# Kernel tuning notes

Hardware: AMD Instinct MI355X
Metric: run time of the kernel (lower is better)

Reference implementation:

```python
import jax, jax.numpy as jnp
import numpy as np

NEG_SLOPE = 0.2


def add_self_loops(edge_index, num_nodes):
    loop = jnp.arange(num_nodes, dtype=edge_index.dtype)
    loops = jnp.stack([loop, loop])  # [2, N]
    return jnp.concatenate([edge_index, loops], axis=1)


def gat_conv(x, edge_index, W, a_src, a_dst, b, concat=True):
    """PyG-style GATConv. a_src/a_dst: [1, H, C]. W: [F_in, H*C]."""
    N = x.shape[0]
    H, C = a_src.shape[1], a_src.shape[2]
    xp = (x @ W).reshape(N, H, C)                       # [N, H, C]
    alpha_src = (xp * a_src).sum(-1)                    # [N, H]
    alpha_dst = (xp * a_dst).sum(-1)                    # [N, H]
    src, dst = edge_index[0], edge_index[1]
    e = alpha_src[src] + alpha_dst[dst]                 # [E, H]
    e = jnp.where(e > 0, e, NEG_SLOPE * e)              # LeakyReLU(0.2)
    # per-destination segment softmax
    m = jax.ops.segment_max(e, dst, num_segments=N)     # [N, H]
    m = jnp.where(jnp.isfinite(m), m, 0.0)
    ez = jnp.exp(e - m[dst])
    s = jax.ops.segment_sum(ez, dst, num_segments=N)    # [N, H]
    alpha = ez / (s[dst] + 1e-16)                       # [E, H]
    msg = xp[src] * alpha[:, :, None]                   # [E, H, C]
    out = jax.ops.segment_sum(msg, dst, num_segments=N) # [N, H, C]
    out = out.reshape(N, H * C) if concat else out.mean(axis=1)
    return out + b


def setup_inputs() -> dict:
    key = jax.random.key(0)
    ks = jax.random.split(key, 16)
    N, F, E, CLS = 100000, 256, 1600000, 10
    x = jax.random.normal(ks[0], (N, F), dtype=jnp.float32)
    edge_index = jax.random.randint(ks[1], (2, E), 0, N, dtype=jnp.int64)

    def glorot(k, shape):
        fan = shape[0] + shape[-1] * (shape[1] if len(shape) == 3 else 1)
        return jax.random.uniform(k, shape, jnp.float32, -1.0, 1.0) * jnp.sqrt(6.0 / fan)

    return {
        "x": x, "edge_index": edge_index,
        "W1": glorot(ks[2], (F, 128)),  "a1s": glorot(ks[3], (1, 8, 16)),
        "a1d": glorot(ks[4], (1, 8, 16)), "b1": jnp.zeros((128,), jnp.float32),
        "W2": glorot(ks[5], (128, 64)), "a2s": glorot(ks[6], (1, 8, 8)),
        "a2d": glorot(ks[7], (1, 8, 8)),  "b2": jnp.zeros((64,), jnp.float32),
        "W3": glorot(ks[8], (64, CLS)), "a3s": glorot(ks[9], (1, 1, CLS)),
        "a3d": glorot(ks[10], (1, 1, CLS)), "b3": jnp.zeros((CLS,), jnp.float32),
    }


def reference(x, edge_index, W1, a1s, a1d, b1, W2, a2s, a2d, b2, W3, a3s, a3d, b3):
    ei = add_self_loops(edge_index, x.shape[0])
    h = jax.nn.elu(gat_conv(x, ei, W1, a1s, a1d, b1))
    h = jax.nn.elu(gat_conv(h, ei, W2, a2s, a2d, b2))
    h = gat_conv(h, ei, W3, a3s, a3d, b3)
    return jax.nn.log_softmax(h, axis=1)
```

## Files before the change

### kernel.cpp

```cpp
#include <hip/hip_runtime.h>
#include <hip/hip_bf16.h>
#include <math.h>


#define LEAKY(v) ((v) > 0.f ? (v) : 0.2f * (v))

typedef __bf16 bf16_t;
typedef __bf16 bf16x8 __attribute__((ext_vector_type(8)));
typedef __bf16 bf16x4 __attribute__((ext_vector_type(4)));
typedef float f32x4 __attribute__((ext_vector_type(4)));
typedef unsigned short u16x8 __attribute__((ext_vector_type(8)));

static __device__ __forceinline__ unsigned short bf_bits(float f) {
    bf16_t b = (bf16_t)f;
    return __builtin_bit_cast(unsigned short, b);
}
static __device__ __forceinline__ float bf_to_f(unsigned short u) {
    return __uint_as_float(((unsigned int)u) << 16);
}
static __device__ __forceinline__ float bperm_f(int byteaddr, float v) {
    return __uint_as_float((unsigned)__builtin_amdgcn_ds_bpermute(byteaddr, (int)__float_as_uint(v)));
}

constexpr int NB_MAX = 400;
constexpr int BCAP = 5120;

__global__ __launch_bounds__(256) void partition_k(
        const int* __restrict__ src, const int* __restrict__ dst, int E, int NB,
        int* __restrict__ bcur, unsigned* __restrict__ staged) {
    __shared__ int hist[NB_MAX];
    __shared__ int bstart[NB_MAX + 1];
    __shared__ int cur[NB_MAX];
    __shared__ int gbase[NB_MAX];
    __shared__ unsigned words[4096];
    __shared__ unsigned short bidl[4096];
    int tid = threadIdx.x;
    int e0 = blockIdx.x * 4096;
    int cnt = E - e0; if (cnt > 4096) cnt = 4096;
    if (cnt <= 0) return;

    for (int b = tid; b < NB; b += 256) hist[b] = 0;
    __syncthreads();
    for (int i = tid; i < cnt; i += 256) atomicAdd(&hist[dst[e0 + i] >> 8], 1);
    __syncthreads();
    if (tid < 64) {
        int lane = tid;
        int run = 0;
        for (int b0 = 0; b0 < NB; b0 += 64) {
            int bb = b0 + lane;
            int v = (bb < NB) ? hist[bb] : 0;
            int sc = v;
            for (int off = 1; off < 64; off <<= 1) {
                int t2 = __shfl_up(sc, off, 64);
                if (lane >= off) sc += t2;
            }
            if (bb < NB) bstart[bb] = run + sc - v;
            run += __shfl(sc, 63, 64);
        }
        if (lane == 0) bstart[NB] = run;
    }
    __syncthreads();
    for (int b = tid; b < NB; b += 256) {
        cur[b] = bstart[b];
        gbase[b] = hist[b] ? atomicAdd(&bcur[b], hist[b]) : 0;
    }
    __syncthreads();
    for (int i = tid; i < cnt; i += 256) {
        int s = src[e0 + i], d = dst[e0 + i];
        int b = d >> 8;
        unsigned w = (unsigned)s | ((unsigned)(d & 255) << 17);
        int p = atomicAdd(&cur[b], 1);
        words[p] = w;
        bidl[p] = (unsigned short)b;
    }
    __syncthreads();
    for (int i = tid; i < cnt; i += 256) {
        int b = bidl[i];
        staged[(size_t)b * BCAP + gbase[b] + (i - bstart[b])] = words[i];
    }
}

__global__ __launch_bounds__(256) void buildcsr_k(
        const unsigned* __restrict__ staged, const int* __restrict__ bcur,
        int* __restrict__ offs, int* __restrict__ cols,
        int N, int NB) {
    __shared__ int h[256], hs[256], curl[256];
    __shared__ int colsl[BCAP];
    __shared__ int base_s;
    int b = blockIdx.x, tid = threadIdx.x;
    int n0 = b << 8;
    int ecnt = bcur[b];
    const unsigned* sb = staged + (size_t)b * BCAP;

    h[tid] = 0;
    if (tid < 64) {
        int acc2 = 0;
        for (int i = tid; i < b; i += 64) acc2 += bcur[i];
        for (int off = 1; off < 64; off <<= 1) acc2 += __shfl_xor(acc2, off, 64);
        if (tid == 0) base_s = acc2;
    }
    __syncthreads();
    int base_g = base_s;
    for (int i = tid; i < ecnt; i += 256) atomicAdd(&h[sb[i] >> 17], 1);
    __syncthreads();
    int val = h[tid];
    hs[tid] = val; __syncthreads();
    for (int off = 1; off < 256; off <<= 1) {
        int t = (tid >= off) ? hs[tid - off] : 0;
        __syncthreads();
        hs[tid] += t;
        __syncthreads();
    }
    int excl = hs[tid] - val;
    curl[tid] = excl;
    if (n0 + tid < N) offs[n0 + tid] = base_g + excl;
    if (b == NB - 1 && tid == 0) offs[N] = base_g + ecnt;
    __syncthreads();
    for (int i = tid; i < ecnt; i += 256) {
        unsigned w = sb[i];
        int p = atomicAdd(&curl[w >> 17], 1);
        colsl[p] = (int)(w & 0x1FFFFu);
    }
    __syncthreads();
    for (int i = tid; i < ecnt; i += 256) cols[base_g + i] = colsl[i];
}

static __device__ __forceinline__ void prep_w_dev(
        const float* __restrict__ W, short* __restrict__ Bfs,
        int K, int N, int NT, int idx) {
    int lane = idx & 63;
    int t = idx >> 6;
    int ntile = t % NT, kstep = t / NT;
    int quad = lane >> 4, nl = lane & 15;
    int n = ntile * 16 + nl;
    bf16_t* dst = (bf16_t*)Bfs + (size_t)idx * 16;
#pragma unroll
    for (int j = 0; j < 8; j++) {
        int k = kstep * 32 + quad * 8 + j;
        float v = W[k * N + n];
        bf16_t h = (bf16_t)v;
        bf16_t l = (bf16_t)(v - (float)h);
        dst[j] = h;
        dst[8 + j] = l;
    }
}
static __device__ __forceinline__ void prep_w3_dev(
        const float* __restrict__ W, short* __restrict__ Bfs, int Nc, int idx) {
    int lane = idx & 63, ks = idx >> 6;
    int quad = lane >> 4, nl = lane & 15;
    bf16_t* dst = (bf16_t*)Bfs + (size_t)idx * 16;
#pragma unroll
    for (int j = 0; j < 8; j++) {
        int k = ks * 32 + quad * 8 + j;
        float v = (nl < Nc) ? W[k * Nc + nl] : 0.f;
        bf16_t h = (bf16_t)v;
        bf16_t l = (bf16_t)(v - (float)h);
        dst[j] = h;
        dst[8 + j] = l;
    }
}
__global__ void prep_all_k(const float* __restrict__ W1, const float* __restrict__ W2,
                           const float* __restrict__ W3, short* __restrict__ Bf1,
                           short* __restrict__ Bf2, short* __restrict__ Bf3) {
    int idx = blockIdx.x * blockDim.x + threadIdx.x;
    if (idx < 4096) prep_w_dev(W1, Bf1, 256, 128, 8, idx);
    else if (idx < 5120) prep_w_dev(W2, Bf2, 128, 64, 4, idx - 4096);
    else if (idx < 5248) prep_w3_dev(W3, Bf3, 10, idx - 5120);
}

template <int BM, int WMT, int WNT, int NWM, bool ABF16, int CHEAD, int K>
__global__ __launch_bounds__(256, 2) void mfma_gemm_k(
        const void* __restrict__ Av, const short* __restrict__ Bfs,
        unsigned short* __restrict__ Cb,
        const float* __restrict__ a_s, const float* __restrict__ a_d,
        float* __restrict__ out_as, float* __restrict__ out_ad,
        int M, int N, int NT) {
    constexpr int NWN = 4 / NWM;
    constexpr int BN = 16 * WNT * NWN;
    constexpr int KP = K + 8;
    constexpr int BNP = BN + 2;
    constexpr size_t ASZ = (size_t)BM * KP * 2 * (ABF16 ? 1 : 2);
    constexpr size_t CSZ = (size_t)BM * BNP * 4;
    constexpr size_t SMEM = ASZ > CSZ ? ASZ : CSZ;
    __shared__ __align__(16) char smem[SMEM];
    bf16_t* As_hi = (bf16_t*)smem;
    bf16_t* As_lo = As_hi + (ABF16 ? 0 : (size_t)BM * KP);
    float* Ct = (float*)smem;
    const bf16_t* Bf = (const bf16_t*)Bfs;

    int tid = threadIdx.x;
    int wave = tid >> 6, lane = tid & 63;
    int quad = lane >> 4, l16 = lane & 15;
    int wm = wave % NWM, wn = wave / NWM;
    int row0 = blockIdx.x * BM;
    int ntile0 = blockIdx.y * (BN / 16) + wn * WNT;

    if constexpr (!ABF16) {
        constexpr int CHUNKS = BM * K * 4 / (16 * 256);
        const float* A = (const float*)Av;
        f32x4 tmp[CHUNKS];
#pragma unroll
        for (int c = 0; c < CHUNKS; c++) {
            int ci = c * 256 + tid;
            int fi = ci * 4;
            int row = fi / K, k = fi % K;
            int grow = row0 + row;
            tmp[c] = (f32x4){0.f, 0.f, 0.f, 0.f};
            if (grow < M) tmp[c] = *(const f32x4*)(A + (size_t)grow * K + k);
        }
#pragma unroll
        for (int c = 0; c < CHUNKS; c++) {
            int ci = c * 256 + tid;
            int fi = ci * 4;
            int row = fi / K, k = fi % K;
            bf16x4 h, l;
#pragma unroll
            for (int j = 0; j < 4; j++) {
                bf16_t hh = (bf16_t)tmp[c][j];
                h[j] = hh;
                l[j] = (bf16_t)(tmp[c][j] - (float)hh);
            }
            *(bf16x4*)&As_hi[row * KP + k] = h;
            *(bf16x4*)&As_lo[row * KP + k] = l;
        }
    } else {
        constexpr int CHUNKS = BM * K * 2 / (16 * 256);
        const unsigned short* A = (const unsigned short*)Av;
        u16x8 tmp[CHUNKS];
#pragma unroll
        for (int c = 0; c < CHUNKS; c++) {
            int ci = c * 256 + tid;
            int ei = ci * 8;
            int row = ei / K, k = ei % K;
            int grow = row0 + row;
            tmp[c] = (u16x8){0, 0, 0, 0, 0, 0, 0, 0};
            if (grow < M) tmp[c] = *(const u16x8*)(A + (size_t)grow * K + k);
        }
#pragma unroll
        for (int c = 0; c < CHUNKS; c++) {
            int ci = c * 256 + tid;
            int ei = ci * 8;
            int row = ei / K, k = ei % K;
            *(u16x8*)&As_hi[row * KP + k] = tmp[c];
        }
    }
    __syncthreads();

    f32x4 acc[WMT][WNT];
#pragma unroll
    for (int i = 0; i < WMT; i++)
#pragma unroll
        for (int j = 0; j < WNT; j++) acc[i][j] = (f32x4){0.f, 0.f, 0.f, 0.f};

#pragma unroll
    for (int ks = 0; ks < K / 32; ks++) {
        bf16x8 ah[WMT], al[WMT];
#pragma unroll
        for (int i = 0; i < WMT; i++) {
            int rowl = wm * (WMT * 16) + i * 16 + l16;
            ah[i] = *(const bf16x8*)&As_hi[rowl * KP + ks * 32 + quad * 8];
            if (!ABF16) al[i] = *(const bf16x8*)&As_lo[rowl * KP + ks * 32 + quad * 8];
        }
        bf16x8 bh[WNT], bl[WNT];
#pragma unroll
        for (int j = 0; j < WNT; j++) {
            size_t base = ((size_t)(ks * NT + ntile0 + j) * 64 + lane) * 16;
            bh[j] = *(const bf16x8*)&Bf[base];
            bl[j] = *(const bf16x8*)&Bf[base + 8];
        }
#pragma unroll
        for (int i = 0; i < WMT; i++)
#pragma unroll
            for (int j = 0; j < WNT; j++) {
                acc[i][j] = __builtin_amdgcn_mfma_f32_16x16x32_bf16(ah[i], bh[j], acc[i][j], 0, 0, 0);
                if (!ABF16)
                    acc[i][j] = __builtin_amdgcn_mfma_f32_16x16x32_bf16(al[i], bh[j], acc[i][j], 0, 0, 0);
                acc[i][j] = __builtin_amdgcn_mfma_f32_16x16x32_bf16(ah[i], bl[j], acc[i][j], 0, 0, 0);
            }
    }

    __syncthreads();
#pragma unroll
    for (int i = 0; i < WMT; i++) {
        int rbase = wm * (WMT * 16) + i * 16 + quad * 4;
#pragma unroll
        for (int j = 0; j < WNT; j++) {
            int lcol = (wn * WNT + j) * 16 + l16;
#pragma unroll
            for (int r2 = 0; r2 < 4; r2++)
                Ct[(size_t)(rbase + r2) * BNP + lcol] = acc[i][j][r2];
        }
    }
    __syncthreads();

    constexpr int HB = BN / CHEAD;
    const int colbase = blockIdx.y * BN;
    const int Hh = N / CHEAD;
#pragma unroll
    for (int o = 0; o < (BM * HB + 255) / 256; o++) {
        int idx = o * 256 + tid;
        if (idx < BM * HB) {
            int row = idx & (BM - 1);
            int hd = idx / BM;
            const float* crow = Ct + (size_t)row * BNP + hd * CHEAD;
            float ss = 0.f, sd = 0.f;
#pragma unroll
            for (int c = 0; c < CHEAD; c++) {
                float v = crow[c];
                ss = fmaf(v, a_s[colbase + hd * CHEAD + c], ss);
                sd = fmaf(v, a_d[colbase + hd * CHEAD + c], sd);
            }
            int grow = row0 + row;
            if (grow < M) {
                out_as[(size_t)grow * Hh + blockIdx.y * HB + hd] = ss;
                out_ad[(size_t)grow * Hh + blockIdx.y * HB + hd] = sd;
            }
        }
    }

    constexpr int CU2 = BM * BN / 2;
#pragma unroll
    for (int o = 0; o < CU2 / 256; o++) {
        int idx = o * 256 + tid;
        int row = idx / (BN / 2);
        int uc = idx - row * (BN / 2);
        float v0 = Ct[(size_t)row * BNP + uc * 2];
        float v1 = Ct[(size_t)row * BNP + uc * 2 + 1];
        unsigned pk = (unsigned)bf_bits(v0) | ((unsigned)bf_bits(v1) << 16);
        int grow = row0 + row;
        if (grow < M)
            ((unsigned*)Cb)[((size_t)grow * N + colbase) / 2 + uc] = pk;
    }
}

__global__ __launch_bounds__(256) void gemm3_k(
        const unsigned short* __restrict__ Ab, const short* __restrict__ Bfs,
        unsigned short* __restrict__ Cb,
        const float* __restrict__ a_s, const float* __restrict__ a_d,
        float* __restrict__ out_as, float* __restrict__ out_ad, int M) {
    const bf16_t* Bf = (const bf16_t*)Bfs;
    int tid = threadIdx.x;
    int wave = tid >> 6, lane = tid & 63;
    int quad = lane >> 4, l16 = lane & 15;
    int grow0 = blockIdx.x * 64 + wave * 16;

    bf16x8 bh[2], bl[2];
#pragma unroll
    for (int ks = 0; ks < 2; ks++) {
        size_t base = (size_t)(ks * 64 + lane) * 16;
        bh[ks] = *(const bf16x8*)&Bf[base];
        bl[ks] = *(const bf16x8*)&Bf[base + 8];
    }

    int arow = grow0 + l16; if (arow >= M) arow = M - 1;
    f32x4 acc = (f32x4){0.f, 0.f, 0.f, 0.f};
#pragma unroll
    for (int ks = 0; ks < 2; ks++) {
        bf16x8 a = *(const bf16x8*)(Ab + (size_t)arow * 64 + ks * 32 + quad * 8);
        acc = __builtin_amdgcn_mfma_f32_16x16x32_bf16(a, bh[ks], acc, 0, 0, 0);
        acc = __builtin_amdgcn_mfma_f32_16x16x32_bf16(a, bl[ks], acc, 0, 0, 0);
    }

    bool colv = l16 < 10;
    float cs = colv ? a_s[l16] : 0.f;
    float cd = colv ? a_d[l16] : 0.f;
    float ps[4], pd[4];
#pragma unroll
    for (int r = 0; r < 4; r++) { ps[r] = acc[r] * cs; pd[r] = acc[r] * cd; }
#pragma unroll
    for (int off = 1; off < 16; off <<= 1) {
#pragma unroll
        for (int r = 0; r < 4; r++) {
            ps[r] += __shfl_xor(ps[r], off, 64);
            pd[r] += __shfl_xor(pd[r], off, 64);
        }
    }
#pragma unroll
    for (int r = 0; r < 4; r++) {
        int grow = grow0 + quad * 4 + r;
        if (grow < M) {
            if (colv) Cb[(size_t)grow * 10 + l16] = bf_bits(acc[r]);
            if (l16 == 0) { out_as[grow] = ps[r]; out_ad[grow] = pd[r]; }
        }
    }
}

template <bool DO_ELU>
__global__ void agg16_k(const unsigned short* __restrict__ xpb,
                        const float* __restrict__ asrc, const float* __restrict__ adst,
                        const int* __restrict__ offs, const int* __restrict__ cols,
                        const float* __restrict__ bias, unsigned short* __restrict__ outb,
                        int N) {
    int gtid = blockIdx.x * blockDim.x + threadIdx.x;
    int n = gtid >> 6;
    if (n >= N) return;
    int lane = threadIdx.x & 63;
    int j = lane >> 3, h = lane & 7;
    const int jb = j << 2;
    int start = offs[n], end = offs[n + 1];
    const unsigned* xp32 = (const unsigned*)xpb;

    unsigned uself = xp32[(size_t)n * 64 + lane];
    float ad_l = adst[n * 8 + h];
    float vs = asrc[n * 8 + h] + ad_l;
    vs = LEAKY(vs);

    float m_w = vs;
    float s = (j == 0) ? 1.f : 0.f;
    float m_f = bperm_f(jb, vs);
    float a0 = __uint_as_float(uself << 16);
    float a1 = __uint_as_float(uself & 0xffff0000u);

    for (int c0 = start; c0 < end; c0 += 16) {
        int e0 = c0 + j, e1 = c0 + 8 + j;
        bool ok0 = e0 < end, ok1 = e1 < end;
        int sl0 = ok0 ? cols[e0] : 0;
        int sl1 = ok1 ? cols[e1] : 0;
        unsigned u[16];
#pragma unroll
        for (int t = 0; t < 8; t++) {
            int srcj = __builtin_amdgcn_readlane(sl0, t * 8);
            u[t] = xp32[(size_t)srcj * 64 + lane];
        }
#pragma unroll
        for (int t = 0; t < 8; t++) {
            int srcj = __builtin_amdgcn_readlane(sl1, t * 8);
            u[8 + t] = xp32[(size_t)srcj * 64 + lane];
        }
        float v0 = -1e30f, v1 = -1e30f;
        if (ok0) { v0 = asrc[sl0 * 8 + h] + ad_l; v0 = LEAKY(v0); }
        if (ok1) { v1 = asrc[sl1 * 8 + h] + ad_l; v1 = LEAKY(v1); }
        float cm = fmaxf(v0, v1);
        cm = fmaxf(cm, __shfl_xor(cm, 8, 64));
        cm = fmaxf(cm, __shfl_xor(cm, 16, 64));
        cm = fmaxf(cm, __shfl_xor(cm, 32, 64));
        float mw_new = fmaxf(m_w, cm);
        float w0 = __expf(v0 - mw_new);
        float w1 = __expf(v1 - mw_new);
        s = s * __expf(m_w - mw_new) + w0 + w1;
        m_w = mw_new;
        float cmF = bperm_f(jb, cm);
        float mf_new = fmaxf(m_f, cmF);
        float scF = __expf(m_f - mf_new);
        m_f = mf_new;
        a0 *= scF; a1 *= scF;
        float wl[16];
#pragma unroll
        for (int t = 0; t < 8; t++) wl[t] = bperm_f(jb + t * 32, w0);
#pragma unroll
        for (int t = 0; t < 8; t++) wl[8 + t] = bperm_f(jb + t * 32, w1);
#pragma unroll
        for (int t = 0; t < 16; t++) {
            a0 = fmaf(wl[t], __uint_as_float(u[t] << 16), a0);
            a1 = fmaf(wl[t], __uint_as_float(u[t] & 0xffff0000u), a1);
        }
    }
    s += __shfl_xor(s, 8, 64);
    s += __shfl_xor(s, 16, 64);
    s += __shfl_xor(s, 32, 64);
    float rs = 1.f / (s + 1e-16f);
    float rsF = bperm_f(jb, rs);
    float o0 = a0 * rsF + bias[2 * lane];
    float o1 = a1 * rsF + bias[2 * lane + 1];
    if (DO_ELU) {
        o0 = o0 > 0.f ? o0 : __expf(o0) - 1.f;
        o1 = o1 > 0.f ? o1 : __expf(o1) - 1.f;
    }
    unsigned packed = (unsigned)bf_bits(o0) | ((unsigned)bf_bits(o1) << 16);
    ((unsigned*)outb)[(size_t)n * 64 + lane] = packed;
}

template <bool DO_ELU>
__global__ void agg8c8_k(const unsigned short* __restrict__ xpb,
                         const float* __restrict__ asrc, const float* __restrict__ adst,
                         const int* __restrict__ offs, const int* __restrict__ cols,
                         const float* __restrict__ bias, unsigned short* __restrict__ outb,
                         int N) {
    int gtid = blockIdx.x * blockDim.x + threadIdx.x;
    int n = gtid >> 6;
    if (n >= N) return;
    int lane = threadIdx.x & 63;
    int j = lane >> 3, h = lane & 7;
    int start = offs[n], end = offs[n + 1];
    const unsigned* xp32 = (const unsigned*)xpb;

    int fp = lane & 31;
    int hF = fp >> 2;
    int half = lane >> 5;
    int sbase = half * 32;

    float ad_l = adst[n * 8 + h];
    float vs = asrc[n * 8 + h] + ad_l;
    vs = LEAKY(vs);

    float m_w = vs;
    float s = (j == 0) ? 1.f : 0.f;
    float m_f = bperm_f(hF * 4, vs);
    float a0 = 0.f, a1 = 0.f;
    if (half == 0) {
        unsigned u = xp32[(size_t)n * 32 + fp];
        a0 = __uint_as_float(u << 16);
        a1 = __uint_as_float(u & 0xffff0000u);
    }

    for (int c0 = start; c0 < end; c0 += 16) {
        int e0 = c0 + j, e1 = c0 + 8 + j;
        bool ok0 = e0 < end, ok1 = e1 < end;
        int sl0 = ok0 ? cols[e0] : 0;
        int sl1 = ok1 ? cols[e1] : 0;
        int sv[8];
#pragma unroll
        for (int t = 0; t < 4; t++) sv[t] = __builtin_amdgcn_ds_bpermute(sbase + t * 64, sl0);
#pragma unroll
        for (int t = 0; t < 4; t++) sv[4 + t] = __builtin_amdgcn_ds_bpermute(sbase + t * 64, sl1);
        unsigned u[8];
#pragma unroll
        for (int t = 0; t < 8; t++) u[t] = xp32[(size_t)sv[t] * 32 + fp];
        float v0 = -1e30f, v1 = -1e30f;
        if (ok0) { v0 = asrc[sl0 * 8 + h] + ad_l; v0 = LEAKY(v0); }
        if (ok1) { v1 = asrc[sl1 * 8 + h] + ad_l; v1 = LEAKY(v1); }
        float cm = fmaxf(v0, v1);
        cm = fmaxf(cm, __shfl_xor(cm, 8, 64));
        cm = fmaxf(cm, __shfl_xor(cm, 16, 64));
        cm = fmaxf(cm, __shfl_xor(cm, 32, 64));
        float mw_new = fmaxf(m_w, cm);
        float w0 = __expf(v0 - mw_new);
        float w1 = __expf(v1 - mw_new);
        s = s * __expf(m_w - mw_new) + w0 + w1;
        m_w = mw_new;
        float cmF = bperm_f(hF * 4, cm);
        float mf_new = fmaxf(m_f, cmF);
        float scF = __expf(m_f - mf_new);
        m_f = mf_new;
        a0 *= scF; a1 *= scF;
        float wl[8];
#pragma unroll
        for (int t = 0; t < 4; t++) wl[t] = bperm_f(sbase + hF * 4 + t * 64, w0);
#pragma unroll
        for (int t = 0; t < 4; t++) wl[4 + t] = bperm_f(sbase + hF * 4 + t * 64, w1);
#pragma unroll
        for (int t = 0; t < 8; t++) {
            a0 = fmaf(wl[t], __uint_as_float(u[t] << 16), a0);
            a1 = fmaf(wl[t], __uint_as_float(u[t] & 0xffff0000u), a1);
        }
    }
    s += __shfl_xor(s, 8, 64);
    s += __shfl_xor(s, 16, 64);
    s += __shfl_xor(s, 32, 64);
    float rs = 1.f / (s + 1e-16f);
    float rsF = bperm_f(hF * 4, rs);
    a0 += __shfl_xor(a0, 32, 64);
    a1 += __shfl_xor(a1, 32, 64);
    if (half == 0) {
        float o0 = a0 * rsF + bias[2 * fp];
        float o1 = a1 * rsF + bias[2 * fp + 1];
        if (DO_ELU) {
            o0 = o0 > 0.f ? o0 : __expf(o0) - 1.f;
            o1 = o1 > 0.f ? o1 : __expf(o1) - 1.f;
        }
        unsigned packed = (unsigned)bf_bits(o0) | ((unsigned)bf_bits(o1) << 16);
        ((unsigned*)outb)[(size_t)n * 32 + fp] = packed;
    }
}

__global__ void agg1h_k(const unsigned short* __restrict__ xpb,
                        const float* __restrict__ asrc, const float* __restrict__ adst,
                        const int* __restrict__ offs, const int* __restrict__ cols,
                        const float* __restrict__ bias, float* __restrict__ out, int N) {
    int gtid = blockIdx.x * blockDim.x + threadIdx.x;
    int n = gtid >> 6;
    if (n >= N) return;
    int lane = threadIdx.x & 63;
    int start = offs[n], end = offs[n + 1];
    float ad = adst[n];
    float vs = asrc[n] + ad;
    vs = LEAKY(vs);

    float m, s;
    if (lane == 0) { m = vs; s = 1.f; } else { m = -1e30f; s = 0.f; }
    for (int e = start + lane; e < end; e += 64) {
        float v = asrc[cols[e]] + ad;
        v = LEAKY(v);
        float mo = fmaxf(m, v);
        s = s * __expf(m - mo) + __expf(v - mo);
        m = mo;
    }
#pragma unroll
    for (int off = 1; off <= 32; off <<= 1) {
        float mo = __shfl_xor(m, off, 64);
        float so = __shfl_xor(s, off, 64);
        float mn = fmaxf(m, mo);
        s = s * __expf(m - mn) + so * __expf(mo - mn);
        m = mn;
    }
    float rs = 1.f / (s + 1e-16f);
    float wself = __expf(vs - m) * rs;

    int j = lane / 10, c = lane - j * 10;
    float acc = 0.f;
    if (j == 0) acc = wself * bf_to_f(xpb[(size_t)n * 10 + c]);
    for (int c0 = start; c0 < end; c0 += 6) {
        int e = c0 + j;
        if (j < 6 && e < end) {
            int src = cols[e];
            float v = asrc[src] + ad;
            v = LEAKY(v);
            float w = __expf(v - m) * rs;
            acc = fmaf(w, bf_to_f(xpb[(size_t)src * 10 + c]), acc);
        }
    }
    float tot = acc;
#pragma unroll
    for (int k = 1; k < 6; k++) tot += __shfl(acc, lane + 10 * k, 64);

    float z = tot + bias[lane < 10 ? lane : 0];
    float mx = -1e30f;
#pragma unroll
    for (int k = 0; k < 10; k++) mx = fmaxf(mx, __shfl(z, k, 64));
    float se = 0.f;
#pragma unroll
    for (int k = 0; k < 10; k++) se += __expf(__shfl(z, k, 64) - mx);
    if (lane < 10) out[(size_t)n * 10 + lane] = z - (__logf(se) + mx);
}


static inline size_t alignup(size_t x) { return (x + 255) & ~(size_t)255; }

extern "C" void kernel_launch(void* const* d_in, const int* in_sizes, int n_in,
                              void* d_out, int out_size, void* d_ws, size_t ws_size,
                              hipStream_t stream) {
    const float* x   = (const float*)d_in[0];
    const int*   ei  = (const int*)d_in[1];
    const float* W1  = (const float*)d_in[2];
    const float* a1s = (const float*)d_in[3];
    const float* a1d = (const float*)d_in[4];
    const float* b1  = (const float*)d_in[5];
    const float* W2  = (const float*)d_in[6];
    const float* a2s = (const float*)d_in[7];
    const float* a2d = (const float*)d_in[8];
    const float* b2  = (const float*)d_in[9];
    const float* W3  = (const float*)d_in[10];
    const float* a3s = (const float*)d_in[11];
    const float* a3d = (const float*)d_in[12];
    const float* b3  = (const float*)d_in[13];
    float* out = (float*)d_out;

    const int N = in_sizes[0] / 256;
    const int E = in_sizes[1] / 2;
    const int* src = ei;
    const int* dst = ei + E;
    const int NB = (N + 255) >> 8;

    char* p = (char*)d_ws;
    int* offs    = (int*)p; p += alignup(sizeof(int) * (size_t)(N + 1));
    int* bcur    = (int*)p; p += alignup(sizeof(int) * (size_t)(NB_MAX + 1));
    int* cols    = (int*)p; p += alignup(sizeof(int) * (size_t)E);
    unsigned short* xpb   = (unsigned short*)p; p += alignup(2 * (size_t)N * 128);
    unsigned short* hbufb = (unsigned short*)p; p += alignup(2 * (size_t)N * 128);
    float* xp    = (float*)p; p += alignup(sizeof(float) * (size_t)N * 128);
    float* as_   = (float*)p; p += alignup(sizeof(float) * (size_t)N * 8);
    float* ad_   = (float*)p; p += alignup(sizeof(float) * (size_t)N * 8);
    short* Bf1   = (short*)p; p += alignup(sizeof(short) * 8 * 8 * 64 * 16);
    short* Bf2   = (short*)p; p += alignup(sizeof(short) * 4 * 4 * 64 * 16);
    short* Bf3   = (short*)p; p += alignup(sizeof(short) * 2 * 1 * 64 * 16);
    unsigned* staged = (unsigned*)xp;

    const int TB = 256;

    hipMemsetAsync(bcur, 0, sizeof(int) * (size_t)(NB + 1), stream);
    partition_k<<<(E + 4095) / 4096, 256, 0, stream>>>(src, dst, E, NB, bcur, staged);
    buildcsr_k<<<NB, 256, 0, stream>>>(staged, bcur, offs, cols, N, NB);

    prep_all_k<<<(5248 + TB - 1) / TB, TB, 0, stream>>>(W1, W2, W3, Bf1, Bf2, Bf3);

    mfma_gemm_k<64, 4, 2, 1, false, 16, 256><<<dim3((N + 63) / 64, 1), 256, 0, stream>>>(
        x, Bf1, xpb, a1s, a1d, as_, ad_, N, 128, 8);
    agg16_k<true><<<(N * 64 + TB - 1) / TB, TB, 0, stream>>>(
        xpb, as_, ad_, offs, cols, b1, hbufb, N);

    mfma_gemm_k<64, 4, 1, 1, true, 8, 128><<<dim3((N + 63) / 64, 1), 256, 0, stream>>>(
        hbufb, Bf2, xpb, a2s, a2d, as_, ad_, N, 64, 4);
    agg8c8_k<true><<<(N * 64 + TB - 1) / TB, TB, 0, stream>>>(
        xpb, as_, ad_, offs, cols, b2, hbufb, N);

    gemm3_k<<<(N + 63) / 64, 256, 0, stream>>>(
        hbufb, Bf3, xpb, a3s, a3d, as_, ad_, N);
    agg1h_k<<<(N * 64 + TB - 1) / TB, TB, 0, stream>>>(
        xpb, as_, ad_, offs, cols, b3, out, N);
}
```

Baseline: 477.2 us.

## Fuse weight prep into partition and CSR build with layer-1 GEMM

Weight-split prep blocks now ride in the partition kernel's launch, and the CSR build blocks share one launch with the layer-1 GEMM blocks, so the two independent jobs overlap and two launches disappear. The layer-1 GEMM stages its A tile in two K-phases, which halves shared memory and allows three blocks per CU. The cost is an extra barrier and reload per phase, and CSR blocks now share a launch with a larger shared-memory footprint.

```diff
diff --git a/kernel.cpp b/kernel.cpp
--- a/kernel.cpp
+++ b/kernel.cpp
@@ -25,9 +25,47 @@
 constexpr int NB_MAX = 400;
 constexpr int BCAP = 5120;
 
-__global__ __launch_bounds__(256) void partition_k(
+static __device__ __forceinline__ void prep_w_dev(
+        const float* __restrict__ W, short* __restrict__ Bfs,
+        int K, int N, int NT, int idx) {
+    int lane = idx & 63;
+    int t = idx >> 6;
+    int ntile = t % NT, kstep = t / NT;
+    int quad = lane >> 4, nl = lane & 15;
+    int n = ntile * 16 + nl;
+    bf16_t* dst = (bf16_t*)Bfs + (size_t)idx * 16;
+#pragma unroll
+    for (int j = 0; j < 8; j++) {
+        int k = kstep * 32 + quad * 8 + j;
+        float v = W[k * N + n];
+        bf16_t h = (bf16_t)v;
+        bf16_t l = (bf16_t)(v - (float)h);
+        dst[j] = h;
+        dst[8 + j] = l;
+    }
+}
+static __device__ __forceinline__ void prep_w3_dev(
+        const float* __restrict__ W, short* __restrict__ Bfs, int Nc, int idx) {
+    int lane = idx & 63, ks = idx >> 6;
+    int quad = lane >> 4, nl = lane & 15;
+    bf16_t* dst = (bf16_t*)Bfs + (size_t)idx * 16;
+#pragma unroll
+    for (int j = 0; j < 8; j++) {
+        int k = ks * 32 + quad * 8 + j;
+        float v = (nl < Nc) ? W[k * Nc + nl] : 0.f;
+        bf16_t h = (bf16_t)v;
+        bf16_t l = (bf16_t)(v - (float)h);
+        dst[j] = h;
+        dst[8 + j] = l;
+    }
+}
+
+__global__ __launch_bounds__(256) void part_prep_k(
         const int* __restrict__ src, const int* __restrict__ dst, int E, int NB,
-        int* __restrict__ bcur, unsigned* __restrict__ staged) {
+        int* __restrict__ bcur, unsigned* __restrict__ staged, int PB,
+        const float* __restrict__ W1, const float* __restrict__ W2,
+        const float* __restrict__ W3, short* __restrict__ Bf1,
+        short* __restrict__ Bf2, short* __restrict__ Bf3) {
     __shared__ int hist[NB_MAX];
     __shared__ int bstart[NB_MAX + 1];
     __shared__ int cur[NB_MAX];
@@ -35,6 +73,15 @@
     __shared__ unsigned words[4096];
     __shared__ unsigned short bidl[4096];
     int tid = threadIdx.x;
+
+    if ((int)blockIdx.x >= PB) {
+        int idx = ((int)blockIdx.x - PB) * 256 + tid;
+        if (idx < 4096) prep_w_dev(W1, Bf1, 256, 128, 8, idx);
+        else if (idx < 5120) prep_w_dev(W2, Bf2, 128, 64, 4, idx - 4096);
+        else if (idx < 5248) prep_w3_dev(W3, Bf3, 10, idx - 5120);
+        return;
+    }
+
     int e0 = blockIdx.x * 4096;
     int cnt = E - e0; if (cnt > 4096) cnt = 4096;
     if (cnt <= 0) return;
@@ -80,14 +127,15 @@
     }
 }
 
-__global__ __launch_bounds__(256) void buildcsr_k(
-        const unsigned* __restrict__ staged, const int* __restrict__ bcur,
-        int* __restrict__ offs, int* __restrict__ cols,
-        int N, int NB) {
-    __shared__ int h[256], hs[256], curl[256];
-    __shared__ int colsl[BCAP];
-    __shared__ int base_s;
-    int b = blockIdx.x, tid = threadIdx.x;
+static __device__ void buildcsr_body(
+        char* smem, const unsigned* __restrict__ staged, const int* __restrict__ bcur,
+        int* __restrict__ offs, int* __restrict__ cols, int N, int NB, int b) {
+    int* h    = (int*)smem;
+    int* hs   = h + 256;
+    int* curl = hs + 256;
+    int* colsl = curl + 256;
+    int* base_p = colsl + BCAP;
+    int tid = threadIdx.x;
     int n0 = b << 8;
     int ecnt = bcur[b];
     const unsigned* sb = staged + (size_t)b * BCAP;
@@ -97,10 +145,10 @@
         int acc2 = 0;
         for (int i = tid; i < b; i += 64) acc2 += bcur[i];
         for (int off = 1; off < 64; off <<= 1) acc2 += __shfl_xor(acc2, off, 64);
-        if (tid == 0) base_s = acc2;
-    }
-    __syncthreads();
-    int base_g = base_s;
+        if (tid == 0) *base_p = acc2;
+    }
+    __syncthreads();
+    int base_g = *base_p;
     for (int i = tid; i < ecnt; i += 256) atomicAdd(&h[sb[i] >> 17], 1);
     __syncthreads();
     int val = h[tid];
@@ -125,66 +173,21 @@
     for (int i = tid; i < ecnt; i += 256) cols[base_g + i] = colsl[i];
 }
 
-static __device__ __forceinline__ void prep_w_dev(
-        const float* __restrict__ W, short* __restrict__ Bfs,
-        int K, int N, int NT, int idx) {
-    int lane = idx & 63;
-    int t = idx >> 6;
-    int ntile = t % NT, kstep = t / NT;
-    int quad = lane >> 4, nl = lane & 15;
-    int n = ntile * 16 + nl;
-    bf16_t* dst = (bf16_t*)Bfs + (size_t)idx * 16;
-#pragma unroll
-    for (int j = 0; j < 8; j++) {
-        int k = kstep * 32 + quad * 8 + j;
-        float v = W[k * N + n];
-        bf16_t h = (bf16_t)v;
-        bf16_t l = (bf16_t)(v - (float)h);
-        dst[j] = h;
-        dst[8 + j] = l;
-    }
-}
-static __device__ __forceinline__ void prep_w3_dev(
-        const float* __restrict__ W, short* __restrict__ Bfs, int Nc, int idx) {
-    int lane = idx & 63, ks = idx >> 6;
-    int quad = lane >> 4, nl = lane & 15;
-    bf16_t* dst = (bf16_t*)Bfs + (size_t)idx * 16;
-#pragma unroll
-    for (int j = 0; j < 8; j++) {
-        int k = ks * 32 + quad * 8 + j;
-        float v = (nl < Nc) ? W[k * Nc + nl] : 0.f;
-        bf16_t h = (bf16_t)v;
-        bf16_t l = (bf16_t)(v - (float)h);
-        dst[j] = h;
-        dst[8 + j] = l;
-    }
-}
-__global__ void prep_all_k(const float* __restrict__ W1, const float* __restrict__ W2,
-                           const float* __restrict__ W3, short* __restrict__ Bf1,
-                           short* __restrict__ Bf2, short* __restrict__ Bf3) {
-    int idx = blockIdx.x * blockDim.x + threadIdx.x;
-    if (idx < 4096) prep_w_dev(W1, Bf1, 256, 128, 8, idx);
-    else if (idx < 5120) prep_w_dev(W2, Bf2, 128, 64, 4, idx - 4096);
-    else if (idx < 5248) prep_w3_dev(W3, Bf3, 10, idx - 5120);
-}
-
-template <int BM, int WMT, int WNT, int NWM, bool ABF16, int CHEAD, int K>
-__global__ __launch_bounds__(256, 2) void mfma_gemm_k(
+template <int BM, int WMT, int WNT, int NWM, bool ABF16, int CHEAD, int K, int NPH>
+static __device__ __forceinline__ void gemm_body(
+        char* smem,
         const void* __restrict__ Av, const short* __restrict__ Bfs,
         unsigned short* __restrict__ Cb,
         const float* __restrict__ a_s, const float* __restrict__ a_d,
         float* __restrict__ out_as, float* __restrict__ out_ad,
-        int M, int N, int NT) {
+        int M, int N, int NT, int bx, int by) {
     constexpr int NWN = 4 / NWM;
     constexpr int BN = 16 * WNT * NWN;
-    constexpr int KP = K + 8;
+    constexpr int KPH = K / NPH;
+    constexpr int KPP = KPH + 8;
     constexpr int BNP = BN + 2;
-    constexpr size_t ASZ = (size_t)BM * KP * 2 * (ABF16 ? 1 : 2);
-    constexpr size_t CSZ = (size_t)BM * BNP * 4;
-    constexpr size_t SMEM = ASZ > CSZ ? ASZ : CSZ;
-    __shared__ __align__(16) char smem[SMEM];
     bf16_t* As_hi = (bf16_t*)smem;
-    bf16_t* As_lo = As_hi + (ABF16 ? 0 : (size_t)BM * KP);
+    bf16_t* As_lo = As_hi + (ABF16 ? 0 : (size_t)BM * KPP);
     float* Ct = (float*)smem;
     const bf16_t* Bf = (const bf16_t*)Bfs;
 
@@ -192,59 +195,8 @@
     int wave = tid >> 6, lane = tid & 63;
     int quad = lane >> 4, l16 = lane & 15;
     int wm = wave % NWM, wn = wave / NWM;
-    int row0 = blockIdx.x * BM;
-    int ntile0 = blockIdx.y * (BN / 16) + wn * WNT;
-
-    if constexpr (!ABF16) {
-        constexpr int CHUNKS = BM * K * 4 / (16 * 256);
-        const float* A = (const float*)Av;
-        f32x4 tmp[CHUNKS];
-#pragma unroll
-        for (int c = 0; c < CHUNKS; c++) {
-            int ci = c * 256 + tid;
-            int fi = ci * 4;
-            int row = fi / K, k = fi % K;
-            int grow = row0 + row;
-            tmp[c] = (f32x4){0.f, 0.f, 0.f, 0.f};
-            if (grow < M) tmp[c] = *(const f32x4*)(A + (size_t)grow * K + k);
-        }
-#pragma unroll
-        for (int c = 0; c < CHUNKS; c++) {
-            int ci = c * 256 + tid;
-            int fi = ci * 4;
-            int row = fi / K, k = fi % K;
-            bf16x4 h, l;
-#pragma unroll
-            for (int j = 0; j < 4; j++) {
-                bf16_t hh = (bf16_t)tmp[c][j];
-                h[j] = hh;
-                l[j] = (bf16_t)(tmp[c][j] - (float)hh);
-            }
-            *(bf16x4*)&As_hi[row * KP + k] = h;
-            *(bf16x4*)&As_lo[row * KP + k] = l;
-        }
-    } else {
-        constexpr int CHUNKS = BM * K * 2 / (16 * 256);
-        const unsigned short* A = (const unsigned short*)Av;
-        u16x8 tmp[CHUNKS];
-#pragma unroll
-        for (int c = 0; c < CHUNKS; c++) {
-            int ci = c * 256 + tid;
-            int ei = ci * 8;
-            int row = ei / K, k = ei % K;
-            int grow = row0 + row;
-            tmp[c] = (u16x8){0, 0, 0, 0, 0, 0, 0, 0};
-            if (grow < M) tmp[c] = *(const u16x8*)(A + (size_t)grow * K + k);
-        }
-#pragma unroll
-        for (int c = 0; c < CHUNKS; c++) {
-            int ci = c * 256 + tid;
-            int ei = ci * 8;
-            int row = ei / K, k = ei % K;
-            *(u16x8*)&As_hi[row * KP + k] = tmp[c];
-        }
-    }
-    __syncthreads();
+    int row0 = bx * BM;
+    int ntile0 = by * (BN / 16) + wn * WNT;
 
     f32x4 acc[WMT][WNT];
 #pragma unroll
@@ -253,30 +205,86 @@
         for (int j = 0; j < WNT; j++) acc[i][j] = (f32x4){0.f, 0.f, 0.f, 0.f};
 
 #pragma unroll
-    for (int ks = 0; ks < K / 32; ks++) {
-        bf16x8 ah[WMT], al[WMT];
-#pragma unroll
-        for (int i = 0; i < WMT; i++) {
-            int rowl = wm * (WMT * 16) + i * 16 + l16;
-            ah[i] = *(const bf16x8*)&As_hi[rowl * KP + ks * 32 + quad * 8];
-            if (!ABF16) al[i] = *(const bf16x8*)&As_lo[rowl * KP + ks * 32 + quad * 8];
-        }
-        bf16x8 bh[WNT], bl[WNT];
-#pragma unroll
-        for (int j = 0; j < WNT; j++) {
-            size_t base = ((size_t)(ks * NT + ntile0 + j) * 64 + lane) * 16;
-            bh[j] = *(const bf16x8*)&Bf[base];
-            bl[j] = *(const bf16x8*)&Bf[base + 8];
-        }
-#pragma unroll
-        for (int i = 0; i < WMT; i++)
+    for (int phase = 0; phase < NPH; phase++) {
+        if (phase) __syncthreads();
+        if constexpr (!ABF16) {
+            constexpr int CHUNKS = BM * KPH * 4 / (16 * 256);
+            const float* A = (const float*)Av;
+            f32x4 tmp[CHUNKS];
+#pragma unroll
+            for (int c = 0; c < CHUNKS; c++) {
+                int ci = c * 256 + tid;
+                int fi = ci * 4;
+                int row = fi / KPH, k = fi % KPH;
+                int grow = row0 + row;
+                tmp[c] = (f32x4){0.f, 0.f, 0.f, 0.f};
+                if (grow < M) tmp[c] = *(const f32x4*)(A + (size_t)grow * K + phase * KPH + k);
+            }
+#pragma unroll
+            for (int c = 0; c < CHUNKS; c++) {
+                int ci = c * 256 + tid;
+                int fi = ci * 4;
+                int row = fi / KPH, k = fi % KPH;
+                bf16x4 h, l;
+#pragma unroll
+                for (int j = 0; j < 4; j++) {
+                    bf16_t hh = (bf16_t)tmp[c][j];
+                    h[j] = hh;
+                    l[j] = (bf16_t)(tmp[c][j] - (float)hh);
+                }
+                *(bf16x4*)&As_hi[row * KPP + k] = h;
+                *(bf16x4*)&As_lo[row * KPP + k] = l;
+            }
+        } else {
+            constexpr int CHUNKS = BM * KPH * 2 / (16 * 256);
+            const unsigned short* A = (const unsigned short*)Av;
+            u16x8 tmp[CHUNKS];
+#pragma unroll
+            for (int c = 0; c < CHUNKS; c++) {
+                int ci = c * 256 + tid;
+                int ei = ci * 8;
+                int row = ei / KPH, k = ei % KPH;
+                int grow = row0 + row;
+                tmp[c] = (u16x8){0, 0, 0, 0, 0, 0, 0, 0};
+                if (grow < M) tmp[c] = *(const u16x8*)(A + (size_t)grow * K + phase * KPH + k);
+            }
+#pragma unroll
+            for (int c = 0; c < CHUNKS; c++) {
+                int ci = c * 256 + tid;
+                int ei = ci * 8;
+                int row = ei / KPH, k = ei % KPH;
+                *(u16x8*)&As_hi[row * KPP + k] = tmp[c];
+            }
+        }
+        __syncthreads();
+
+#pragma unroll
+        for (int ks = 0; ks < KPH / 32; ks++) {
+            int ksg = phase * (KPH / 32) + ks;
+            bf16x8 ah[WMT], al[WMT];
+#pragma unroll
+            for (int i = 0; i < WMT; i++) {
+                int rowl = wm * (WMT * 16) + i * 16 + l16;
+                ah[i] = *(const bf16x8*)&As_hi[rowl * KPP + ks * 32 + quad * 8];
+                if (!ABF16) al[i] = *(const bf16x8*)&As_lo[rowl * KPP + ks * 32 + quad * 8];
+            }
+            bf16x8 bh[WNT], bl[WNT];
 #pragma unroll
             for (int j = 0; j < WNT; j++) {
-                acc[i][j] = __builtin_amdgcn_mfma_f32_16x16x32_bf16(ah[i], bh[j], acc[i][j], 0, 0, 0);
-                if (!ABF16)
-                    acc[i][j] = __builtin_amdgcn_mfma_f32_16x16x32_bf16(al[i], bh[j], acc[i][j], 0, 0, 0);
-                acc[i][j] = __builtin_amdgcn_mfma_f32_16x16x32_bf16(ah[i], bl[j], acc[i][j], 0, 0, 0);
-            }
+                size_t base = ((size_t)(ksg * NT + ntile0 + j) * 64 + lane) * 16;
+                bh[j] = *(const bf16x8*)&Bf[base];
+                bl[j] = *(const bf16x8*)&Bf[base + 8];
+            }
+#pragma unroll
+            for (int i = 0; i < WMT; i++)
+#pragma unroll
+                for (int j = 0; j < WNT; j++) {
+                    acc[i][j] = __builtin_amdgcn_mfma_f32_16x16x32_bf16(ah[i], bh[j], acc[i][j], 0, 0, 0);
+                    if (!ABF16)
+                        acc[i][j] = __builtin_amdgcn_mfma_f32_16x16x32_bf16(al[i], bh[j], acc[i][j], 0, 0, 0);
+                    acc[i][j] = __builtin_amdgcn_mfma_f32_16x16x32_bf16(ah[i], bl[j], acc[i][j], 0, 0, 0);
+                }
+        }
     }
 
     __syncthreads();
@@ -294,7 +302,7 @@
     __syncthreads();
 
     constexpr int HB = BN / CHEAD;
-    const int colbase = blockIdx.y * BN;
+    const int colbase = by * BN;
     const int Hh = N / CHEAD;
 #pragma unroll
     for (int o = 0; o < (BM * HB + 255) / 256; o++) {
@@ -312,8 +320,8 @@
             }
             int grow = row0 + row;
             if (grow < M) {
-                out_as[(size_t)grow * Hh + blockIdx.y * HB + hd] = ss;
-                out_ad[(size_t)grow * Hh + blockIdx.y * HB + hd] = sd;
+                out_as[(size_t)grow * Hh + by * HB + hd] = ss;
+                out_ad[(size_t)grow * Hh + by * HB + hd] = sd;
             }
         }
     }
@@ -331,6 +339,35 @@
         if (grow < M)
             ((unsigned*)Cb)[((size_t)grow * N + colbase) / 2 + uc] = pk;
     }
+}
+
+constexpr int SMEM1 = 64 * (128 + 8) * 2 * 2;
+__global__ __launch_bounds__(256, 3) void csr_gemm1_k(
+        const unsigned* __restrict__ staged, const int* __restrict__ bcur,
+        int* __restrict__ offs, int* __restrict__ cols, int Nn, int NB,
+        const float* __restrict__ x, const short* __restrict__ Bf1,
+        unsigned short* __restrict__ xpb,
+        const float* __restrict__ a1s, const float* __restrict__ a1d,
+        float* __restrict__ out_as, float* __restrict__ out_ad, int M) {
+    __shared__ __align__(16) char smem[SMEM1];
+    if ((int)blockIdx.x < NB) {
+        buildcsr_body(smem, staged, bcur, offs, cols, Nn, NB, blockIdx.x);
+    } else {
+        gemm_body<64, 4, 2, 1, false, 16, 256, 2>(
+            smem, x, Bf1, xpb, a1s, a1d, out_as, out_ad, M, 128, 8,
+            (int)blockIdx.x - NB, 0);
+    }
+}
+
+constexpr int SMEM2 = 64 * (128 + 8) * 2;
+__global__ __launch_bounds__(256, 2) void mfma_gemm2_k(
+        const unsigned short* __restrict__ Ab, const short* __restrict__ Bf2,
+        unsigned short* __restrict__ Cb,
+        const float* __restrict__ a_s, const float* __restrict__ a_d,
+        float* __restrict__ out_as, float* __restrict__ out_ad, int M) {
+    __shared__ __align__(16) char smem[SMEM2];
+    gemm_body<64, 4, 1, 1, true, 8, 128, 1>(
+        smem, Ab, Bf2, Cb, a_s, a_d, out_as, out_ad, M, 64, 4, blockIdx.x, 0);
 }
 
 __global__ __launch_bounds__(256) void gemm3_k(
@@ -650,6 +687,7 @@
     const int* src = ei;
     const int* dst = ei + E;
     const int NB = (N + 255) >> 8;
+    const int PB = (E + 4095) / 4096;
 
     char* p = (char*)d_ws;
     int* offs    = (int*)p; p += alignup(sizeof(int) * (size_t)(N + 1));
@@ -668,18 +706,16 @@
     const int TB = 256;
 
     hipMemsetAsync(bcur, 0, sizeof(int) * (size_t)(NB + 1), stream);
-    partition_k<<<(E + 4095) / 4096, 256, 0, stream>>>(src, dst, E, NB, bcur, staged);
-    buildcsr_k<<<NB, 256, 0, stream>>>(staged, bcur, offs, cols, N, NB);
-
-    prep_all_k<<<(5248 + TB - 1) / TB, TB, 0, stream>>>(W1, W2, W3, Bf1, Bf2, Bf3);
-
-    mfma_gemm_k<64, 4, 2, 1, false, 16, 256><<<dim3((N + 63) / 64, 1), 256, 0, stream>>>(
-        x, Bf1, xpb, a1s, a1d, as_, ad_, N, 128, 8);
+    part_prep_k<<<PB + 21, 256, 0, stream>>>(
+        src, dst, E, NB, bcur, staged, PB, W1, W2, W3, Bf1, Bf2, Bf3);
+
+    csr_gemm1_k<<<NB + (N + 63) / 64, 256, 0, stream>>>(
+        staged, bcur, offs, cols, N, NB, x, Bf1, xpb, a1s, a1d, as_, ad_, N);
     agg16_k<true><<<(N * 64 + TB - 1) / TB, TB, 0, stream>>>(
         xpb, as_, ad_, offs, cols, b1, hbufb, N);
 
-    mfma_gemm_k<64, 4, 1, 1, true, 8, 128><<<dim3((N + 63) / 64, 1), 256, 0, stream>>>(
-        hbufb, Bf2, xpb, a2s, a2d, as_, ad_, N, 64, 4);
+    mfma_gemm2_k<<<(N + 63) / 64, 256, 0, stream>>>(
+        hbufb, Bf2, xpb, a2s, a2d, as_, ad_, N);
     agg8c8_k<true><<<(N * 64 + TB - 1) / TB, TB, 0, stream>>>(
         xpb, as_, ad_, offs, cols, b2, hbufb, N);
 
```

Result: faster. 456.9 us (-4.2%).
